# Optimization experiments

Measured on AMD Instinct MI355X. Metric: run time of the kernel, lower is better.

The kernel has to match this reference:

```python
import jax, jax.numpy as jnp
import numpy as np

VOCAB, EMBED, NFEAT, T, HIDDEN, NCLASS, BATCH = 50000, 50, 3, 120, 300, 5, 1024
D_IN = NFEAT * EMBED  # 150


def setup_inputs() -> dict:
    key = jax.random.key(0)
    ks = jax.random.split(key, 5)
    s_in = 1.0 / np.sqrt(D_IN)
    s_h = 1.0 / np.sqrt(HIDDEN)
    return {
        "ids": jax.random.randint(ks[0], (BATCH, T, NFEAT), 0, VOCAB, dtype=jnp.int32),
        "embed": jax.random.normal(ks[1], (VOCAB, EMBED), dtype=jnp.float32),
        "Wx": jax.random.normal(ks[2], (D_IN, 4 * HIDDEN), dtype=jnp.float32) * s_in,
        "Wh": jax.random.normal(ks[3], (HIDDEN, 4 * HIDDEN), dtype=jnp.float32) * s_h,
        "b": jnp.zeros((4 * HIDDEN,), dtype=jnp.float32),
        "U": jax.random.normal(ks[4], (HIDDEN, NCLASS), dtype=jnp.float32) * s_h,
        "b2": jnp.zeros((NCLASS,), dtype=jnp.float32),
    }


def reference(ids, embed, Wx, Wh, b, U, b2):
    # Embedding lookup + concat windows: (B, T, 3) -> (B, T, 150)
    x = embed[ids].reshape(ids.shape[0], T, D_IN)
    # Precompute input contribution for all timesteps: (B, T, 4H)
    xz = jnp.einsum("btd,dg->btg", x, Wx) + b
    xz = jnp.transpose(xz, (1, 0, 2))  # (T, B, 4H)

    def step(carry, xz_t):
        c, h = carry
        z = xz_t + h @ Wh  # (B, 4H)
        i, f, g, o = jnp.split(z, 4, axis=-1)
        i = jax.nn.sigmoid(i)
        f = jax.nn.sigmoid(f)
        o = jax.nn.sigmoid(o)
        g = jnp.tanh(g)
        c = f * c + i * g
        h = o * jnp.tanh(c)
        # dropout at inference (keep_prob=1) is identity
        y = h @ U + b2  # (B, C)
        return (c, h), y

    B = ids.shape[0]
    init = (jnp.zeros((B, HIDDEN), x.dtype), jnp.zeros((B, HIDDEN), x.dtype))
    _, ys = jax.lax.scan(step, init, xz)  # ys: (T, B, C)
    return jnp.transpose(ys, (1, 0, 2))  # (B, T, C)
```

## Files before the change

kernel.cpp:

```cpp
#include <hip/hip_runtime.h>


#define BATCH 1024
#define TT    120
#define HID   300
#define KX    160
#define KH    320
#define SL    64
#define HSL   60
#define NCOL  1280
#define GH    5
#define GB    32
#define BS    32
#define XST   168
#define FSTR  32
#define NSLOT 3
#define NB    256
#define NREL  (GH * 4)

typedef __attribute__((ext_vector_type(8))) short bf16x8;
typedef __attribute__((ext_vector_type(4))) float f32x4;

__device__ __forceinline__ unsigned short f2b(float f) {
  union { float f; unsigned u; } v; v.f = f;
  unsigned r = v.u + 0x7fffu + ((v.u >> 16) & 1u);
  return (unsigned short)(r >> 16);
}
__device__ __forceinline__ float sigm(float x) {
  return __builtin_amdgcn_rcpf(1.f + __expf(-x));
}
__device__ __forceinline__ float tanhf_(float x) {
  return 2.f * __builtin_amdgcn_rcpf(1.f + __expf(-2.f * x)) - 1.f;
}

__global__ void k_reorder_wh(const float* __restrict__ W, unsigned short* __restrict__ Wp) {
  int tid = blockIdx.x * 256 + threadIdx.x;
  if (tid >= KH * NCOL) return;
  int c = tid % NCOL, k = tid / NCOL;
  int js = k >> 6, v0 = k & 63;
  int j = c >> 8, r = c & 255, g = r >> 6, u0 = r & 63;
  float val = 0.f;
  if (v0 < HSL && u0 < HSL) val = W[(js * HSL + v0) * 1200 + g * 300 + j * HSL + u0];
  Wp[((k >> 3) * NCOL + c) * 8 + (k & 7)] = f2b(val);
}

__global__ void k_reorder_wx(const float* __restrict__ W, unsigned short* __restrict__ Wp) {
  int tid = blockIdx.x * 256 + threadIdx.x;
  if (tid >= KX * NCOL) return;
  int c = tid % NCOL, k = tid / NCOL;
  int j = c >> 8, r = c & 255, g = r >> 6, u0 = r & 63;
  float val = 0.f;
  if (k < 150 && u0 < HSL) val = W[k * 1200 + g * 300 + j * HSL + u0];
  Wp[((k >> 3) * NCOL + c) * 8 + (k & 7)] = f2b(val);
}

__global__ void k_reorder_b(const float* __restrict__ b, float* __restrict__ bp) {
  int c = blockIdx.x * 256 + threadIdx.x;
  if (c >= NCOL) return;
  int j = c >> 8, r = c & 255, g = r >> 6, u0 = r & 63;
  bp[c] = (u0 < HSL) ? b[g * 300 + j * HSL + u0] : 0.f;
}

__global__ void k_reorder_u(const float* __restrict__ U, unsigned short* __restrict__ Up) {
  int tid = blockIdx.x * 256 + threadIdx.x;
  if (tid >= KH * 16) return;
  int n = tid % 16, k = tid / 16;
  int js = k >> 6, v0 = k & 63;
  float v = (v0 < HSL && n < 5) ? U[(js * HSL + v0) * 5 + n] : 0.f;
  Up[((k >> 3) * 16 + n) * 8 + (k & 7)] = f2b(v);
}

__launch_bounds__(256, 1)
__attribute__((amdgpu_waves_per_eu(1, 1)))
__global__ void k_lstm(const int* __restrict__ ids, const float* __restrict__ embed,
                       const unsigned short* __restrict__ Wp,
                       const unsigned short* __restrict__ Wxp,
                       const float* __restrict__ bp,
                       const unsigned short* __restrict__ Up,
                       unsigned short* __restrict__ hbuf,
                       int* __restrict__ flags,
                       int* __restrict__ xcd_cnt,
                       const float* __restrict__ b2,
                       float* __restrict__ out) {
  __shared__ __align__(16) unsigned short x_lds[2][BS * XST];
  __shared__ char lds_pad[61440];
  __shared__ int role[2];

  const int tid = threadIdx.x;
  if (tid == 0) {
    ((volatile char*)lds_pad)[0] = 0;
    int xcd = __builtin_amdgcn_s_getreg(63508) & 7;
    int rank = atomicAdd(&xcd_cnt[xcd], 1);
    role[0] = xcd; role[1] = rank;
  }
  __syncthreads();
  const int xcd = role[0], rank = role[1];
  if (rank >= GH * 4) return;
  const int bg = xcd * 4 + rank / GH;
  const int j  = rank % GH;

  const int lane = tid & 63, w = tid >> 6;
  const int l15 = lane & 15, l4 = lane >> 4;

  if (tid < BS) {
#pragma unroll
    for (int bq = 0; bq < 2; ++bq)
      for (int e = 150; e < XST; ++e) x_lds[bq][tid * XST + e] = 0;
  }

  const int colb = j * 256 + w * 16 + l15;

  bf16x8 bh[10][4], bx[5][4];
#pragma unroll
  for (int kk = 0; kk < 10; ++kk)
#pragma unroll
    for (int g = 0; g < 4; ++g)
      bh[kk][g] = *(const bf16x8*)(Wp + ((kk * 4 + l4) * NCOL + colb + g * 64) * 8);
#pragma unroll
  for (int kk = 0; kk < 5; ++kk)
#pragma unroll
    for (int g = 0; g < 4; ++g)
      bx[kk][g] = *(const bf16x8*)(Wxp + ((kk * 4 + l4) * NCOL + colb + g * 64) * 8);

  float bias[4];
#pragma unroll
  for (int g = 0; g < 4; ++g) bias[g] = bp[colb + g * 64];
  const float b2v = (l15 < 5) ? b2[l15] : 0.f;

  int xrow = 0, koff = 0, nf2 = 0, f = 0;
  const bool gth = (tid < 192);
  if (gth) {
    xrow = tid / 6; int half = tid % 6; f = half >> 1; int hh = half & 1;
    nf2 = hh ? 12 : 13;
    koff = f * 50 + (hh ? 26 : 0);
  }
  const long idbase = (long)(bg * BS + xrow) * TT * 3 + f;
  const int  eoff   = (koff - f * 50);

  if (gth) {
    int id0 = ids[idbase + 0 * 3];
    const float* src = embed + (long)id0 * 50 + eoff;
    unsigned short* dst = &x_lds[0][xrow * XST + koff];
#pragma unroll
    for (int e = 0; e < 13; ++e)
      if (e < nf2) {
        float2 v = *(const float2*)(src + 2 * e);
        *(unsigned*)(dst + 2 * e) = (unsigned)f2b(v.x) | ((unsigned)f2b(v.y) << 16);
      }
  }
  __syncthreads();

  f32x4 acc[4][2];
  float cst[2][4];
#pragma unroll
  for (int g = 0; g < 4; ++g)
#pragma unroll
    for (int mt = 0; mt < 2; ++mt) acc[g][mt] = {0.f, 0.f, 0.f, 0.f};
#pragma unroll
  for (int mt = 0; mt < 2; ++mt)
#pragma unroll
    for (int r = 0; r < 4; ++r) cst[mt][r] = 0.f;

  {
    const unsigned short* xb = &x_lds[0][l15 * XST + l4 * 8];
#pragma unroll
    for (int kk = 0; kk < 5; ++kk) {
      bf16x8 a0 = *(const bf16x8*)(xb + kk * 32);
      bf16x8 a1 = *(const bf16x8*)(xb + 16 * XST + kk * 32);
#pragma unroll
      for (int g = 0; g < 4; ++g) {
        acc[g][0] = __builtin_amdgcn_mfma_f32_16x16x32_bf16(a0, bx[kk][g], acc[g][0], 0, 0, 0);
        acc[g][1] = __builtin_amdgcn_mfma_f32_16x16x32_bf16(a1, bx[kk][g], acc[g][1], 0, 0, 0);
      }
    }
  }

  float2 xv[13];
  int idv = 0;
  if (gth) {
    int id1 = ids[idbase + 1 * 3];
    const float* src = embed + (long)id1 * 50 + eoff;
#pragma unroll
    for (int e = 0; e < 13; ++e)
      if (e < nf2) xv[e] = *(const float2*)(src + 2 * e);
    idv = ids[idbase + 2 * 3];
  }

  bf16x8 va0[10], va1[10];

  for (int t = 0; t < TT; ++t) {
    if (t > 0) {
      const int* fp = flags + ((t - 1) * GB + bg) * FSTR;
      int it = 0;
      while (__hip_atomic_load(fp, __ATOMIC_RELAXED, __HIP_MEMORY_SCOPE_AGENT) < NREL) {
        if (++it > 300000) break;
      }
      asm volatile("buffer_inv\n\ts_waitcnt vmcnt(0)" ::: "memory");

      const unsigned short* ar =
          hbuf + ((t - 1) % NSLOT) * (BATCH * KH) + (bg * BS + l15) * KH + l4 * 8;
#pragma unroll
      for (int kk = 0; kk < 10; ++kk) {
        va0[kk] = *(const bf16x8*)(ar + kk * 32);
        va1[kk] = *(const bf16x8*)(ar + 16 * KH + kk * 32);
      }
#pragma unroll
      for (int kk = 0; kk < 10; ++kk) {
#pragma unroll
        for (int g = 0; g < 4; ++g) {
          acc[g][0] = __builtin_amdgcn_mfma_f32_16x16x32_bf16(va0[kk], bh[kk][g], acc[g][0], 0, 0, 0);
          acc[g][1] = __builtin_amdgcn_mfma_f32_16x16x32_bf16(va1[kk], bh[kk][g], acc[g][1], 0, 0, 0);
        }
      }
    }

    unsigned short* hdst = hbuf + (t % NSLOT) * (BATCH * KH);
#pragma unroll
    for (int mt = 0; mt < 2; ++mt) {
#pragma unroll
      for (int r = 0; r < 4; ++r) {
        float zi = acc[0][mt][r] + bias[0];
        float zf = acc[1][mt][r] + bias[1];
        float zg = acc[2][mt][r] + bias[2];
        float zo = acc[3][mt][r] + bias[3];
        float gi = sigm(zi), gf = sigm(zf), go = sigm(zo), gg = tanhf_(zg);
        float c = gf * cst[mt][r] + gi * gg;
        cst[mt][r] = c;
        float h = go * tanhf_(c);
        unsigned v = f2b(h);
        unsigned p1 = v | ((unsigned)__shfl_xor((int)v, 1) << 16);
        unsigned long long p2 = (unsigned long long)p1 |
            ((unsigned long long)(unsigned)__shfl_xor((int)p1, 2) << 32);
        if ((l15 & 3) == 0) {
          int row = bg * BS + mt * 16 + l4 * 4 + r;
          *(unsigned long long*)(hdst + row * KH + j * SL + w * 16 + l15) = p2;
        }
      }
      acc[0][mt] = {0.f, 0.f, 0.f, 0.f};
      acc[1][mt] = {0.f, 0.f, 0.f, 0.f};
      acc[2][mt] = {0.f, 0.f, 0.f, 0.f};
      acc[3][mt] = {0.f, 0.f, 0.f, 0.f};
    }

    asm volatile("s_waitcnt vmcnt(0)" ::: "memory");
    if ((tid & 63) == 0)
      __hip_atomic_fetch_add(flags + (t * GB + bg) * FSTR, 1, __ATOMIC_RELAXED,
                             __HIP_MEMORY_SCOPE_AGENT);

    if (t > 0 && j == (t - 1) % GH) {
      if (w == 2) {
        f32x4 ay = {0.f, 0.f, 0.f, 0.f};
#pragma unroll
        for (int kk = 0; kk < 10; ++kk) {
          bf16x8 u = *(const bf16x8*)(Up + ((kk * 4 + l4) * 16 + l15) * 8);
          ay = __builtin_amdgcn_mfma_f32_16x16x32_bf16(va0[kk], u, ay, 0, 0, 0);
        }
        if (l15 < 5)
#pragma unroll
          for (int q = 0; q < 4; ++q)
            out[((bg * BS + l4 * 4 + q) * TT + (t - 1)) * 5 + l15] = ay[q] + b2v;
      } else if (w == 3) {
        f32x4 ay = {0.f, 0.f, 0.f, 0.f};
#pragma unroll
        for (int kk = 0; kk < 10; ++kk) {
          bf16x8 u = *(const bf16x8*)(Up + ((kk * 4 + l4) * 16 + l15) * 8);
          ay = __builtin_amdgcn_mfma_f32_16x16x32_bf16(va1[kk], u, ay, 0, 0, 0);
        }
        if (l15 < 5)
#pragma unroll
          for (int q = 0; q < 4; ++q)
            out[((bg * BS + 16 + l4 * 4 + q) * TT + (t - 1)) * 5 + l15] = ay[q] + b2v;
      }
    }

    if (t + 1 < TT) {
      if (gth) {
        unsigned short* dst = &x_lds[(t + 1) & 1][xrow * XST + koff];
#pragma unroll
        for (int e = 0; e < 13; ++e)
          if (e < nf2)
            *(unsigned*)(dst + 2 * e) = (unsigned)f2b(xv[e].x) | ((unsigned)f2b(xv[e].y) << 16);
      }
      __syncthreads();
      const unsigned short* xb = &x_lds[(t + 1) & 1][l15 * XST + l4 * 8];
#pragma unroll
      for (int kk = 0; kk < 5; ++kk) {
        bf16x8 a0 = *(const bf16x8*)(xb + kk * 32);
        bf16x8 a1 = *(const bf16x8*)(xb + 16 * XST + kk * 32);
#pragma unroll
        for (int g = 0; g < 4; ++g) {
          acc[g][0] = __builtin_amdgcn_mfma_f32_16x16x32_bf16(a0, bx[kk][g], acc[g][0], 0, 0, 0);
          acc[g][1] = __builtin_amdgcn_mfma_f32_16x16x32_bf16(a1, bx[kk][g], acc[g][1], 0, 0, 0);
        }
      }
      if (gth && t + 2 < TT) {
        const float* src = embed + (long)idv * 50 + eoff;
#pragma unroll
        for (int e = 0; e < 13; ++e)
          if (e < nf2) xv[e] = *(const float2*)(src + 2 * e);
        if (t + 3 < TT) idv = ids[idbase + (long)(t + 3) * 3];
      }
    }
  }

  if (j == (TT - 1) % GH) {
    const int* fp = flags + ((TT - 1) * GB + bg) * FSTR;
    int it = 0;
    while (__hip_atomic_load(fp, __ATOMIC_RELAXED, __HIP_MEMORY_SCOPE_AGENT) < NREL) {
      if (++it > 300000) break;
    }
    asm volatile("buffer_inv\n\ts_waitcnt vmcnt(0)" ::: "memory");
    const unsigned short* ar =
        hbuf + ((TT - 1) % NSLOT) * (BATCH * KH) + (bg * BS + l15) * KH + l4 * 8;
#pragma unroll
    for (int kk = 0; kk < 10; ++kk) {
      va0[kk] = *(const bf16x8*)(ar + kk * 32);
      va1[kk] = *(const bf16x8*)(ar + 16 * KH + kk * 32);
    }
    if (w == 2) {
      f32x4 ay = {0.f, 0.f, 0.f, 0.f};
#pragma unroll
      for (int kk = 0; kk < 10; ++kk) {
        bf16x8 u = *(const bf16x8*)(Up + ((kk * 4 + l4) * 16 + l15) * 8);
        ay = __builtin_amdgcn_mfma_f32_16x16x32_bf16(va0[kk], u, ay, 0, 0, 0);
      }
      if (l15 < 5)
#pragma unroll
        for (int q = 0; q < 4; ++q)
          out[((bg * BS + l4 * 4 + q) * TT + (TT - 1)) * 5 + l15] = ay[q] + b2v;
    } else if (w == 3) {
      f32x4 ay = {0.f, 0.f, 0.f, 0.f};
#pragma unroll
      for (int kk = 0; kk < 10; ++kk) {
        bf16x8 u = *(const bf16x8*)(Up + ((kk * 4 + l4) * 16 + l15) * 8);
        ay = __builtin_amdgcn_mfma_f32_16x16x32_bf16(va1[kk], u, ay, 0, 0, 0);
      }
      if (l15 < 5)
#pragma unroll
        for (int q = 0; q < 4; ++q)
          out[((bg * BS + 16 + l4 * 4 + q) * TT + (TT - 1)) * 5 + l15] = ay[q] + b2v;
    }
  }
}

extern "C" void kernel_launch(void* const* d_in, const int* in_sizes, int n_in,
                              void* d_out, int out_size, void* d_ws, size_t ws_size,
                              hipStream_t stream) {
  const int*   ids   = (const int*)d_in[0];
  const float* embed = (const float*)d_in[1];
  const float* Wx    = (const float*)d_in[2];
  const float* Wh    = (const float*)d_in[3];
  const float* b     = (const float*)d_in[4];
  const float* U     = (const float*)d_in[5];
  const float* b2    = (const float*)d_in[6];
  float* out = (float*)d_out;

  char* ws = (char*)d_ws;
  size_t off = 0;
  unsigned short* Wp   = (unsigned short*)(ws + off); off += (size_t)KH * NCOL * 2;
  unsigned short* Wxp  = (unsigned short*)(ws + off); off += (size_t)KX * NCOL * 2;
  float*          bp   = (float*)(ws + off);          off += (size_t)NCOL * 4;
  unsigned short* Up   = (unsigned short*)(ws + off); off += (size_t)KH * 16 * 2;
  unsigned short* hbuf = (unsigned short*)(ws + off); off += (size_t)NSLOT * BATCH * KH * 2;
  int*            flags= (int*)(ws + off);            off += (size_t)TT * GB * FSTR * 4;
  int*            xcd_cnt = (int*)(ws + off);         off += 8 * 4;
  if (ws_size < off) return;

  hipMemsetAsync(flags, 0, TT * GB * FSTR * 4 + 8 * 4, stream);
  k_reorder_wh<<<(KH * NCOL + 255) / 256, 256, 0, stream>>>(Wh, Wp);
  k_reorder_wx<<<(KX * NCOL + 255) / 256, 256, 0, stream>>>(Wx, Wxp);
  k_reorder_b<<<(NCOL + 255) / 256, 256, 0, stream>>>(b, bp);
  k_reorder_u<<<(KH * 16 + 255) / 256, 256, 0, stream>>>(U, Up);

  k_lstm<<<dim3(NB), dim3(256), 0, stream>>>(ids, embed, Wp, Wxp, bp, Up,
                                             hbuf, flags, xcd_cnt, b2, out);
}
```

Baseline: 711.8 us.

## Double threads per LSTM block and exchange gate pre-activations through LDS

Launches the persistent LSTM kernel with 512 threads instead of 256, so each wave owns one 16-row M tile and a gate-pair slice. Gate pre-activations are staged in LDS so that elementwise cell updates are redistributed across threads. Flag waiting is done by a single thread with s_sleep and a block barrier, and each block increments the flag once instead of once per wave. The memset is replaced by an init kernel. The aim is more MFMA parallelism per CU and less spinning traffic, at the cost of extra LDS round trips and block-wide barriers on every timestep.

```diff
diff --git a/kernel.cpp b/kernel.cpp
--- a/kernel.cpp
+++ b/kernel.cpp
@@ -16,7 +16,7 @@
 #define FSTR  32
 #define NSLOT 3
 #define NB    256
-#define NREL  (GH * 4)
+#define THR   512
 
 typedef __attribute__((ext_vector_type(8))) short bf16x8;
 typedef __attribute__((ext_vector_type(4))) float f32x4;
@@ -70,8 +70,15 @@
   Up[((k >> 3) * 16 + n) * 8 + (k & 7)] = f2b(v);
 }
 
-__launch_bounds__(256, 1)
-__attribute__((amdgpu_waves_per_eu(1, 1)))
+__global__ void k_init(int* __restrict__ flags, int n, int* __restrict__ xcd_cnt) {
+  int i = blockIdx.x * 256 + threadIdx.x;
+  if (i < n)
+    __hip_atomic_store(flags + i, 0, __ATOMIC_RELAXED, __HIP_MEMORY_SCOPE_AGENT);
+  if (i < 8)
+    __hip_atomic_store(xcd_cnt + i, 0, __ATOMIC_RELAXED, __HIP_MEMORY_SCOPE_AGENT);
+}
+
+__launch_bounds__(THR, 2)
 __global__ void k_lstm(const int* __restrict__ ids, const float* __restrict__ embed,
                        const unsigned short* __restrict__ Wp,
                        const unsigned short* __restrict__ Wxp,
@@ -83,6 +90,7 @@
                        const float* __restrict__ b2,
                        float* __restrict__ out) {
   __shared__ __align__(16) unsigned short x_lds[2][BS * XST];
+  __shared__ __align__(16) float z_lds[BS * 4 * SL];
   __shared__ char lds_pad[61440];
   __shared__ int role[2];
 
@@ -100,6 +108,9 @@
   const int j  = rank % GH;
 
   const int lane = tid & 63, w = tid >> 6;
+  const int wm = w >> 2;
+  const int gp = (w >> 1) & 1;
+  const int uh = w & 1;
   const int l15 = lane & 15, l4 = lane >> 4;
 
   if (tid < BS) {
@@ -108,23 +119,29 @@
       for (int e = 150; e < XST; ++e) x_lds[bq][tid * XST + e] = 0;
   }
 
-  const int colb = j * 256 + w * 16 + l15;
-
   bf16x8 bh[10][4], bx[5][4];
 #pragma unroll
   for (int kk = 0; kk < 10; ++kk)
 #pragma unroll
-    for (int g = 0; g < 4; ++g)
-      bh[kk][g] = *(const bf16x8*)(Wp + ((kk * 4 + l4) * NCOL + colb + g * 64) * 8);
+    for (int gf = 0; gf < 4; ++gf) {
+      int col = j * 256 + (2 * gp + (gf >> 1)) * 64 + uh * 32 + (gf & 1) * 16 + l15;
+      bh[kk][gf] = *(const bf16x8*)(Wp + ((kk * 4 + l4) * NCOL + col) * 8);
+    }
 #pragma unroll
   for (int kk = 0; kk < 5; ++kk)
 #pragma unroll
-    for (int g = 0; g < 4; ++g)
-      bx[kk][g] = *(const bf16x8*)(Wxp + ((kk * 4 + l4) * NCOL + colb + g * 64) * 8);
-
-  float bias[4];
-#pragma unroll
-  for (int g = 0; g < 4; ++g) bias[g] = bp[colb + g * 64];
+    for (int gf = 0; gf < 4; ++gf) {
+      int col = j * 256 + (2 * gp + (gf >> 1)) * 64 + uh * 32 + (gf & 1) * 16 + l15;
+      bx[kk][gf] = *(const bf16x8*)(Wxp + ((kk * 4 + l4) * NCOL + col) * 8);
+    }
+
+  const int grow = tid >> 4, gup = tid & 15;
+  float bias[4][4];
+#pragma unroll
+  for (int g = 0; g < 4; ++g)
+#pragma unroll
+    for (int i = 0; i < 4; ++i)
+      bias[g][i] = bp[j * 256 + g * 64 + gup * 4 + i];
   const float b2v = (l15 < 5) ? b2[l15] : 0.f;
 
   int xrow = 0, koff = 0, nf2 = 0, f = 0;
@@ -150,28 +167,21 @@
   }
   __syncthreads();
 
-  f32x4 acc[4][2];
-  float cst[2][4];
-#pragma unroll
-  for (int g = 0; g < 4; ++g)
-#pragma unroll
-    for (int mt = 0; mt < 2; ++mt) acc[g][mt] = {0.f, 0.f, 0.f, 0.f};
-#pragma unroll
-  for (int mt = 0; mt < 2; ++mt)
-#pragma unroll
-    for (int r = 0; r < 4; ++r) cst[mt][r] = 0.f;
+  f32x4 acc[4];
+  float cst[4];
+#pragma unroll
+  for (int gf = 0; gf < 4; ++gf) acc[gf] = {0.f, 0.f, 0.f, 0.f};
+#pragma unroll
+  for (int i = 0; i < 4; ++i) cst[i] = 0.f;
 
   {
-    const unsigned short* xb = &x_lds[0][l15 * XST + l4 * 8];
+    const unsigned short* xb = &x_lds[0][(wm * 16 + l15) * XST + l4 * 8];
 #pragma unroll
     for (int kk = 0; kk < 5; ++kk) {
-      bf16x8 a0 = *(const bf16x8*)(xb + kk * 32);
-      bf16x8 a1 = *(const bf16x8*)(xb + 16 * XST + kk * 32);
-#pragma unroll
-      for (int g = 0; g < 4; ++g) {
-        acc[g][0] = __builtin_amdgcn_mfma_f32_16x16x32_bf16(a0, bx[kk][g], acc[g][0], 0, 0, 0);
-        acc[g][1] = __builtin_amdgcn_mfma_f32_16x16x32_bf16(a1, bx[kk][g], acc[g][1], 0, 0, 0);
-      }
+      bf16x8 a = *(const bf16x8*)(xb + kk * 32);
+#pragma unroll
+      for (int gf = 0; gf < 4; ++gf)
+        acc[gf] = __builtin_amdgcn_mfma_f32_16x16x32_bf16(a, bx[kk][gf], acc[gf], 0, 0, 0);
     }
   }
 
@@ -186,91 +196,82 @@
     idv = ids[idbase + 2 * 3];
   }
 
-  bf16x8 va0[10], va1[10];
+  bf16x8 va[10];
 
   for (int t = 0; t < TT; ++t) {
     if (t > 0) {
-      const int* fp = flags + ((t - 1) * GB + bg) * FSTR;
-      int it = 0;
-      while (__hip_atomic_load(fp, __ATOMIC_RELAXED, __HIP_MEMORY_SCOPE_AGENT) < NREL) {
-        if (++it > 300000) break;
-      }
+      if (tid == 0) {
+        int* fp = flags + ((t - 1) * GB + bg) * FSTR;
+        int it = 0;
+        while (__hip_atomic_load(fp, __ATOMIC_RELAXED, __HIP_MEMORY_SCOPE_AGENT) < GH) {
+          __builtin_amdgcn_s_sleep(1);
+          if (++it > 200000) break;
+        }
+      }
+      __syncthreads();
       asm volatile("buffer_inv\n\ts_waitcnt vmcnt(0)" ::: "memory");
 
       const unsigned short* ar =
-          hbuf + ((t - 1) % NSLOT) * (BATCH * KH) + (bg * BS + l15) * KH + l4 * 8;
-#pragma unroll
-      for (int kk = 0; kk < 10; ++kk) {
-        va0[kk] = *(const bf16x8*)(ar + kk * 32);
-        va1[kk] = *(const bf16x8*)(ar + 16 * KH + kk * 32);
-      }
-#pragma unroll
-      for (int kk = 0; kk < 10; ++kk) {
-#pragma unroll
-        for (int g = 0; g < 4; ++g) {
-          acc[g][0] = __builtin_amdgcn_mfma_f32_16x16x32_bf16(va0[kk], bh[kk][g], acc[g][0], 0, 0, 0);
-          acc[g][1] = __builtin_amdgcn_mfma_f32_16x16x32_bf16(va1[kk], bh[kk][g], acc[g][1], 0, 0, 0);
-        }
-      }
-    }
-
-    unsigned short* hdst = hbuf + (t % NSLOT) * (BATCH * KH);
-#pragma unroll
-    for (int mt = 0; mt < 2; ++mt) {
-#pragma unroll
-      for (int r = 0; r < 4; ++r) {
-        float zi = acc[0][mt][r] + bias[0];
-        float zf = acc[1][mt][r] + bias[1];
-        float zg = acc[2][mt][r] + bias[2];
-        float zo = acc[3][mt][r] + bias[3];
-        float gi = sigm(zi), gf = sigm(zf), go = sigm(zo), gg = tanhf_(zg);
-        float c = gf * cst[mt][r] + gi * gg;
-        cst[mt][r] = c;
-        float h = go * tanhf_(c);
-        unsigned v = f2b(h);
-        unsigned p1 = v | ((unsigned)__shfl_xor((int)v, 1) << 16);
-        unsigned long long p2 = (unsigned long long)p1 |
-            ((unsigned long long)(unsigned)__shfl_xor((int)p1, 2) << 32);
-        if ((l15 & 3) == 0) {
-          int row = bg * BS + mt * 16 + l4 * 4 + r;
-          *(unsigned long long*)(hdst + row * KH + j * SL + w * 16 + l15) = p2;
-        }
-      }
-      acc[0][mt] = {0.f, 0.f, 0.f, 0.f};
-      acc[1][mt] = {0.f, 0.f, 0.f, 0.f};
-      acc[2][mt] = {0.f, 0.f, 0.f, 0.f};
-      acc[3][mt] = {0.f, 0.f, 0.f, 0.f};
+          hbuf + ((t - 1) % NSLOT) * (BATCH * KH) + (bg * BS + wm * 16 + l15) * KH + l4 * 8;
+#pragma unroll
+      for (int kk = 0; kk < 10; ++kk)
+        va[kk] = *(const bf16x8*)(ar + kk * 32);
+#pragma unroll
+      for (int kk = 0; kk < 10; ++kk)
+#pragma unroll
+        for (int gf = 0; gf < 4; ++gf)
+          acc[gf] = __builtin_amdgcn_mfma_f32_16x16x32_bf16(va[kk], bh[kk][gf], acc[gf], 0, 0, 0);
+    }
+
+#pragma unroll
+    for (int gf = 0; gf < 4; ++gf) {
+      int gate = 2 * gp + (gf >> 1);
+      int uu = uh * 32 + (gf & 1) * 16 + l15;
+#pragma unroll
+      for (int r = 0; r < 4; ++r)
+        z_lds[(wm * 16 + l4 * 4 + r) * 256 + gate * 64 + uu] = acc[gf][r];
+      acc[gf] = {0.f, 0.f, 0.f, 0.f};
+    }
+    __syncthreads();
+
+    {
+      const float* zr = z_lds + grow * 256 + gup * 4;
+      unsigned short hsv[4];
+#pragma unroll
+      for (int i = 0; i < 4; ++i) {
+        float zi = zr[0 * 64 + i] + bias[0][i];
+        float zf = zr[1 * 64 + i] + bias[1][i];
+        float zg = zr[2 * 64 + i] + bias[2][i];
+        float zo = zr[3 * 64 + i] + bias[3][i];
+        float gi = sigm(zi), gf_ = sigm(zf), go = sigm(zo), gg = tanhf_(zg);
+        float c = gf_ * cst[i] + gi * gg;
+        cst[i] = c;
+        hsv[i] = f2b(go * tanhf_(c));
+      }
+      unsigned long long p2 =
+          (unsigned long long)((unsigned)hsv[0] | ((unsigned)hsv[1] << 16)) |
+          ((unsigned long long)((unsigned)hsv[2] | ((unsigned)hsv[3] << 16)) << 32);
+      unsigned short* hdst = hbuf + (t % NSLOT) * (BATCH * KH);
+      *(unsigned long long*)(hdst + (bg * BS + grow) * KH + j * SL + gup * 4) = p2;
     }
 
     asm volatile("s_waitcnt vmcnt(0)" ::: "memory");
-    if ((tid & 63) == 0)
+    __syncthreads();
+    if (tid == 0)
       __hip_atomic_fetch_add(flags + (t * GB + bg) * FSTR, 1, __ATOMIC_RELAXED,
                              __HIP_MEMORY_SCOPE_AGENT);
 
-    if (t > 0 && j == (t - 1) % GH) {
-      if (w == 2) {
-        f32x4 ay = {0.f, 0.f, 0.f, 0.f};
-#pragma unroll
-        for (int kk = 0; kk < 10; ++kk) {
-          bf16x8 u = *(const bf16x8*)(Up + ((kk * 4 + l4) * 16 + l15) * 8);
-          ay = __builtin_amdgcn_mfma_f32_16x16x32_bf16(va0[kk], u, ay, 0, 0, 0);
-        }
-        if (l15 < 5)
-#pragma unroll
-          for (int q = 0; q < 4; ++q)
-            out[((bg * BS + l4 * 4 + q) * TT + (t - 1)) * 5 + l15] = ay[q] + b2v;
-      } else if (w == 3) {
-        f32x4 ay = {0.f, 0.f, 0.f, 0.f};
-#pragma unroll
-        for (int kk = 0; kk < 10; ++kk) {
-          bf16x8 u = *(const bf16x8*)(Up + ((kk * 4 + l4) * 16 + l15) * 8);
-          ay = __builtin_amdgcn_mfma_f32_16x16x32_bf16(va1[kk], u, ay, 0, 0, 0);
-        }
-        if (l15 < 5)
-#pragma unroll
-          for (int q = 0; q < 4; ++q)
-            out[((bg * BS + 16 + l4 * 4 + q) * TT + (t - 1)) * 5 + l15] = ay[q] + b2v;
-      }
+    if (t > 0 && j == (t - 1) % GH && (w & 3) == 0) {
+      f32x4 ay = {0.f, 0.f, 0.f, 0.f};
+#pragma unroll
+      for (int kk = 0; kk < 10; ++kk) {
+        bf16x8 u = *(const bf16x8*)(Up + ((kk * 4 + l4) * 16 + l15) * 8);
+        ay = __builtin_amdgcn_mfma_f32_16x16x32_bf16(va[kk], u, ay, 0, 0, 0);
+      }
+      if (l15 < 5)
+#pragma unroll
+        for (int q = 0; q < 4; ++q)
+          out[((bg * BS + wm * 16 + l4 * 4 + q) * TT + (t - 1)) * 5 + l15] = ay[q] + b2v;
     }
 
     if (t + 1 < TT) {
@@ -282,16 +283,13 @@
             *(unsigned*)(dst + 2 * e) = (unsigned)f2b(xv[e].x) | ((unsigned)f2b(xv[e].y) << 16);
       }
       __syncthreads();
-      const unsigned short* xb = &x_lds[(t + 1) & 1][l15 * XST + l4 * 8];
+      const unsigned short* xb = &x_lds[(t + 1) & 1][(wm * 16 + l15) * XST + l4 * 8];
 #pragma unroll
       for (int kk = 0; kk < 5; ++kk) {
-        bf16x8 a0 = *(const bf16x8*)(xb + kk * 32);
-        bf16x8 a1 = *(const bf16x8*)(xb + 16 * XST + kk * 32);
-#pragma unroll
-        for (int g = 0; g < 4; ++g) {
-          acc[g][0] = __builtin_amdgcn_mfma_f32_16x16x32_bf16(a0, bx[kk][g], acc[g][0], 0, 0, 0);
-          acc[g][1] = __builtin_amdgcn_mfma_f32_16x16x32_bf16(a1, bx[kk][g], acc[g][1], 0, 0, 0);
-        }
+        bf16x8 a = *(const bf16x8*)(xb + kk * 32);
+#pragma unroll
+        for (int gf = 0; gf < 4; ++gf)
+          acc[gf] = __builtin_amdgcn_mfma_f32_16x16x32_bf16(a, bx[kk][gf], acc[gf], 0, 0, 0);
       }
       if (gth && t + 2 < TT) {
         const float* src = embed + (long)idv * 50 + eoff;
@@ -304,41 +302,32 @@
   }
 
   if (j == (TT - 1) % GH) {
-    const int* fp = flags + ((TT - 1) * GB + bg) * FSTR;
-    int it = 0;
-    while (__hip_atomic_load(fp, __ATOMIC_RELAXED, __HIP_MEMORY_SCOPE_AGENT) < NREL) {
-      if (++it > 300000) break;
-    }
+    if (tid == 0) {
+      int* fp = flags + ((TT - 1) * GB + bg) * FSTR;
+      int it = 0;
+      while (__hip_atomic_load(fp, __ATOMIC_RELAXED, __HIP_MEMORY_SCOPE_AGENT) < GH) {
+        __builtin_amdgcn_s_sleep(1);
+        if (++it > 200000) break;
+      }
+    }
+    __syncthreads();
     asm volatile("buffer_inv\n\ts_waitcnt vmcnt(0)" ::: "memory");
-    const unsigned short* ar =
-        hbuf + ((TT - 1) % NSLOT) * (BATCH * KH) + (bg * BS + l15) * KH + l4 * 8;
-#pragma unroll
-    for (int kk = 0; kk < 10; ++kk) {
-      va0[kk] = *(const bf16x8*)(ar + kk * 32);
-      va1[kk] = *(const bf16x8*)(ar + 16 * KH + kk * 32);
-    }
-    if (w == 2) {
+    if ((w & 3) == 0) {
+      const unsigned short* ar =
+          hbuf + ((TT - 1) % NSLOT) * (BATCH * KH) + (bg * BS + wm * 16 + l15) * KH + l4 * 8;
+#pragma unroll
+      for (int kk = 0; kk < 10; ++kk)
+        va[kk] = *(const bf16x8*)(ar + kk * 32);
       f32x4 ay = {0.f, 0.f, 0.f, 0.f};
 #pragma unroll
       for (int kk = 0; kk < 10; ++kk) {
         bf16x8 u = *(const bf16x8*)(Up + ((kk * 4 + l4) * 16 + l15) * 8);
-        ay = __builtin_amdgcn_mfma_f32_16x16x32_bf16(va0[kk], u, ay, 0, 0, 0);
+        ay = __builtin_amdgcn_mfma_f32_16x16x32_bf16(va[kk], u, ay, 0, 0, 0);
       }
       if (l15 < 5)
 #pragma unroll
         for (int q = 0; q < 4; ++q)
-          out[((bg * BS + l4 * 4 + q) * TT + (TT - 1)) * 5 + l15] = ay[q] + b2v;
-    } else if (w == 3) {
-      f32x4 ay = {0.f, 0.f, 0.f, 0.f};
-#pragma unroll
-      for (int kk = 0; kk < 10; ++kk) {
-        bf16x8 u = *(const bf16x8*)(Up + ((kk * 4 + l4) * 16 + l15) * 8);
-        ay = __builtin_amdgcn_mfma_f32_16x16x32_bf16(va1[kk], u, ay, 0, 0, 0);
-      }
-      if (l15 < 5)
-#pragma unroll
-        for (int q = 0; q < 4; ++q)
-          out[((bg * BS + 16 + l4 * 4 + q) * TT + (TT - 1)) * 5 + l15] = ay[q] + b2v;
+          out[((bg * BS + wm * 16 + l4 * 4 + q) * TT + (TT - 1)) * 5 + l15] = ay[q] + b2v;
     }
   }
 }
@@ -366,12 +355,12 @@
   int*            xcd_cnt = (int*)(ws + off);         off += 8 * 4;
   if (ws_size < off) return;
 
-  hipMemsetAsync(flags, 0, TT * GB * FSTR * 4 + 8 * 4, stream);
+  k_init<<<(TT * GB * FSTR + 255) / 256, 256, 0, stream>>>(flags, TT * GB * FSTR, xcd_cnt);
   k_reorder_wh<<<(KH * NCOL + 255) / 256, 256, 0, stream>>>(Wh, Wp);
   k_reorder_wx<<<(KX * NCOL + 255) / 256, 256, 0, stream>>>(Wx, Wxp);
   k_reorder_b<<<(NCOL + 255) / 256, 256, 0, stream>>>(b, bp);
   k_reorder_u<<<(KH * 16 + 255) / 256, 256, 0, stream>>>(U, Up);
 
-  k_lstm<<<dim3(NB), dim3(256), 0, stream>>>(ids, embed, Wp, Wxp, bp, Up,
+  k_lstm<<<dim3(NB), dim3(THR), 0, stream>>>(ids, embed, Wp, Wxp, bp, Up,
                                              hbuf, flags, xcd_cnt, b2, out);
 }
```

Measured after the change: 1.772 ms. 149% more time.
